# Optimization experiments

Hardware: AMD Instinct MI355X
Metric: run time of the kernel (lower is better)

## Reference

```python
import jax, jax.numpy as jnp
import numpy as np

HEADS = 16

def setup_inputs() -> dict:
    key = jax.random.key(0)
    k1, k2, k3 = jax.random.split(key, 3)
    B, S, D = 4, 2048, 1024
    x = jax.random.normal(k1, (B, S, D), dtype=jnp.float32)
    w_qkv = jax.random.normal(k2, (D, 3 * D), dtype=jnp.float32) * (D ** -0.5)
    w_out = jax.random.normal(k3, (D, D), dtype=jnp.float32) * (D ** -0.5)
    return {"x": x, "w_qkv": w_qkv, "w_out": w_out}

def reference(x, w_qkv, w_out):
    B, S, D = x.shape
    H = HEADS
    hd = D // H
    qkv = jnp.einsum("bsd,de->bse", x, w_qkv)  # [B,S,3D]
    q, k, v = jnp.split(qkv, 3, axis=-1)
    # [B,S,D] -> [B,H,S,hd]
    q = q.reshape(B, S, H, hd).transpose(0, 2, 1, 3)
    k = k.reshape(B, S, H, hd).transpose(0, 2, 1, 3)
    v = v.reshape(B, S, H, hd).transpose(0, 2, 1, 3)
    scores = jnp.einsum("bhqd,bhkd->bhqk", q, k) / jnp.sqrt(jnp.float32(hd))
    attn = jax.nn.softmax(scores, axis=-1)
    out = jnp.einsum("bhqk,bhkd->bhqd", attn, v)  # [B,H,S,hd]
    out = out.transpose(0, 2, 1, 3).reshape(B, S, D)
    return jnp.einsum("bsd,de->bse", out, w_out)
```

## Files before the change

### kernel.cpp

```cpp
#include <hip/hip_runtime.h>

typedef __bf16 bf16;
typedef __bf16 bfx8 __attribute__((ext_vector_type(8)));
typedef __bf16 bfx4 __attribute__((ext_vector_type(4)));
typedef float f32x4 __attribute__((ext_vector_type(4)));

#define MFMA_BF16 __builtin_amdgcn_mfma_f32_16x16x32_bf16

static constexpr int Bq = 4, Sq = 2048, Dq = 1024, Hq = 16, HDq = 64;
static constexpr int Mq = Bq * Sq;
static constexpr int D3 = 3 * Dq;
static constexpr int NQK = 2 * Dq;
static constexpr float L2E = 1.4426950408889634f;
static constexpr float QSC = 0.125f * L2E;

typedef const __attribute__((address_space(1))) void* gas1;
typedef __attribute__((address_space(3))) void* las3;

__device__ __forceinline__ void gload_lds16(const bf16* g, bf16* l) {
    __builtin_amdgcn_global_load_lds((gas1)g, (las3)l, 16, 0, 0);
}

__device__ __forceinline__ float fast_exp2(float x) {
    return __builtin_amdgcn_exp2f(x);
}

__global__ __launch_bounds__(256) void prep(const float* __restrict__ x,
                                            const float* __restrict__ w_qkv,
                                            const float* __restrict__ w_out,
                                            bf16* __restrict__ x_bf,
                                            bf16* __restrict__ wqkvT,
                                            bf16* __restrict__ woutT) {
    __shared__ float tile[32][33];
    int bid = blockIdx.x, tid = threadIdx.x;
    if (bid < 8192) {
        int i = (bid * 256 + tid) * 4;
        float4 v = *(const float4*)(x + i);
        bfx4 r;
        r[0] = (bf16)v.x; r[1] = (bf16)v.y; r[2] = (bf16)v.z; r[3] = (bf16)v.w;
        *(bfx4*)(x_bf + i) = r;
        return;
    }
    const float* in; bf16* out; int R, C, blk;
    if (bid < 8192 + 3072) { blk = bid - 8192;  in = w_qkv; out = wqkvT; R = Dq; C = D3; }
    else                   { blk = bid - 11264; in = w_out; out = woutT; R = Dq; C = Dq; }
    int tx = tid & 31, ty = tid >> 5;
    int nbx = C / 32;
    int c0 = (blk % nbx) * 32, r0 = (blk / nbx) * 32;
    for (int j = 0; j < 32; j += 8)
        tile[ty + j][tx] = in[(size_t)(r0 + ty + j) * C + c0 + tx];
    __syncthreads();
    for (int j = 0; j < 32; j += 8)
        out[(size_t)(c0 + ty + j) * R + r0 + tx] = (bf16)tile[tx][ty + j];
}

__device__ __forceinline__ int ldsb(int d, int s) {
    return d * 256 + ((((s >> 3) ^ (d & 15)) << 4) | ((s & 7) * 2));
}

__device__ __forceinline__ void stage_tile(const bf16* A, const bf16* Bt,
                                           bf16* As, bf16* Bs,
                                           int m0, int n0, int K, int k0, int tid) {
    #pragma unroll
    for (int i = 0; i < 4; i++) {
        int c = i * 256 + tid;
        int row = c >> 3;
        int ch = (c & 7) ^ (row & 7);
        gload_lds16(A + (size_t)(m0 + row) * K + k0 + ch * 8, As + c * 8);
        gload_lds16(Bt + (size_t)(n0 + row) * K + k0 + ch * 8, Bs + c * 8);
    }
}

template <bool OUT_F32, bool QSCALE, bool VSPLIT>
__global__ __launch_bounds__(256) void gemm_bt(const bf16* __restrict__ A,
                                               const bf16* __restrict__ Bt,
                                               void* __restrict__ Cout,
                                               bf16* __restrict__ Vout,
                                               int M, int N, int K) {
    __shared__ bf16 smem[4 * 8192];
    int m0 = blockIdx.y * 128;
    int n0 = blockIdx.x * 128;
    int tid = threadIdx.x;
    int lane = tid & 63, wave = tid >> 6;
    int quad = lane >> 4, l16 = lane & 15;
    int wr = wave >> 1, wc = wave & 1;
    int sw = l16 & 7;

    f32x4 acc[4][4] = {};

    stage_tile(A, Bt, smem, smem + 8192, m0, n0, K, 0, tid);
    asm volatile("s_waitcnt vmcnt(0)" ::: "memory");
    __builtin_amdgcn_s_barrier();

    int nt = K >> 6;
    #pragma unroll 1
    for (int t = 0; t < nt; t++) {
        int cur = t & 1;
        if (t + 1 < nt)
            stage_tile(A, Bt, smem + (cur ^ 1) * 16384, smem + (cur ^ 1) * 16384 + 8192,
                       m0, n0, K, (t + 1) * 64, tid);
        const bf16* As = smem + cur * 16384;
        const bf16* Bs = As + 8192;
        #pragma unroll
        for (int s = 0; s < 2; s++) {
            bfx8 af[4], bfr[4];
            #pragma unroll
            for (int i = 0; i < 4; i++)
                af[i] = *(const bfx8*)(As + (wr * 64 + i * 16 + l16) * 64 +
                                       ((s * 4 + quad) ^ sw) * 8);
            #pragma unroll
            for (int j = 0; j < 4; j++)
                bfr[j] = *(const bfx8*)(Bs + (wc * 64 + j * 16 + l16) * 64 +
                                        ((s * 4 + quad) ^ sw) * 8);
            #pragma unroll
            for (int i = 0; i < 4; i++)
                #pragma unroll
                for (int j = 0; j < 4; j++)
                    acc[i][j] = MFMA_BF16(af[i], bfr[j], acc[i][j], 0, 0, 0);
        }
        asm volatile("s_waitcnt vmcnt(0)" ::: "memory");
        __builtin_amdgcn_s_barrier();
    }

    if (VSPLIT && n0 >= NQK) {
        #pragma unroll
        for (int i = 0; i < 4; i++)
            #pragma unroll
            for (int j = 0; j < 4; j++) {
                int d = wc * 64 + j * 16 + l16;
                int s0 = wr * 64 + i * 16 + quad * 4;
                bfx4 pv;
                #pragma unroll
                for (int r = 0; r < 4; r++) pv[r] = (bf16)acc[i][j][r];
                *(bfx4*)((char*)smem + ldsb(d, s0)) = pv;
            }
        __syncthreads();
        int b = m0 >> 11, st = m0 & (Sq - 1), d0 = n0 - NQK;
        int g = (lane >> 3) & 1, t8 = lane & 7;
        int ss = g * 64 + (t8 >> 2) * 32 + (t8 & 3) * 4;
        #pragma unroll
        for (int rep = 0; rep < 8; rep++) {
            int d = wave * 4 + (lane >> 4) + rep * 16;
            bfx4 lo = *(const bfx4*)((char*)smem + ldsb(d, ss));
            bfx4 hi = *(const bfx4*)((char*)smem + ldsb(d, ss + 16));
            bfx8 o8;
            #pragma unroll
            for (int r = 0; r < 4; r++) { o8[r] = lo[r]; o8[4 + r] = hi[r]; }
            *(bfx8*)(Vout + ((size_t)b * Dq + d0 + d) * Sq + st + g * 64 + t8 * 8) = o8;
        }
        return;
    }

    #pragma unroll
    for (int i = 0; i < 4; i++)
        #pragma unroll
        for (int j = 0; j < 4; j++) {
            int col = n0 + wc * 64 + j * 16 + l16;
            int cstride = VSPLIT ? NQK : N;
            float scale = (QSCALE && col < Dq) ? QSC : 1.0f;
            #pragma unroll
            for (int r = 0; r < 4; r++) {
                int row = m0 + wr * 64 + i * 16 + quad * 4 + r;
                if (OUT_F32)
                    ((float*)Cout)[(size_t)row * cstride + col] = acc[i][j][r];
                else
                    ((bf16*)Cout)[(size_t)row * cstride + col] = (bf16)(acc[i][j][r] * scale);
            }
        }
}

__global__ __launch_bounds__(256, 4) void attn_kernel(const bf16* __restrict__ qkv,
                                                      const bf16* __restrict__ Vt,
                                                      bf16* __restrict__ out) {
    __shared__ bf16 Ks[3][64 * 64];
    __shared__ bf16 Vs[2][64 * 64];

    int bid = blockIdx.x;
    int qc = (bid >> 3) & 15;
    int head = ((bid >> 7) << 3) | (bid & 7);
    int h = head & 15, b = head >> 4;
    int tid = threadIdx.x;
    int lane = tid & 63, wave = tid >> 6;
    int quad = lane >> 4, l16 = lane & 15;
    int sw = l16 & 7;

    size_t base = (size_t)b * Sq * NQK;
    const bf16* Kbase = qkv + base + Dq + h * HDq;
    const bf16* Vbase = Vt + ((size_t)b * Dq + h * HDq) * Sq;
    int q0 = qc * 128 + wave * 32;

    bfx8 qf[2][2];
    #pragma unroll
    for (int qt = 0; qt < 2; qt++)
        #pragma unroll
        for (int s = 0; s < 2; s++)
            qf[qt][s] = *(const bfx8*)(qkv + base + (size_t)(q0 + qt * 16 + l16) * NQK +
                                       h * HDq + s * 32 + quad * 8);

    bfx8 ones;
    #pragma unroll
    for (int j = 0; j < 8; j++) ones[j] = (bf16)1.0f;

    f32x4 oacc[2][4] = {};
    f32x4 lacc[2] = {};

    int c0 = tid, c1 = tid + 256;
    int r0 = c0 >> 3, ch0 = (c0 & 7) ^ (r0 & 7);
    int r1 = c1 >> 3, ch1 = (c1 & 7) ^ (r1 & 7);

    bf16 *kC = Ks[0], *kN = Ks[1], *kF = Ks[2];
    bf16 *vC = Vs[0], *vN = Vs[1];

    gload_lds16(Kbase + (size_t)r0 * NQK + ch0 * 8, kC + c0 * 8);
    gload_lds16(Kbase + (size_t)r1 * NQK + ch1 * 8, kC + c1 * 8);
    gload_lds16(Vbase + (size_t)r0 * Sq + ch0 * 8, vC + c0 * 8);
    gload_lds16(Vbase + (size_t)r1 * Sq + ch1 * 8, vC + c1 * 8);
    gload_lds16(Kbase + (size_t)(64 + r0) * NQK + ch0 * 8, kN + c0 * 8);
    gload_lds16(Kbase + (size_t)(64 + r1) * NQK + ch1 * 8, kN + c1 * 8);

    #pragma unroll 1
    for (int i = 0; i < 32; i++) {
        if (i < 31) asm volatile("s_waitcnt vmcnt(2)" ::: "memory");
        else        asm volatile("s_waitcnt vmcnt(0)" ::: "memory");
        __builtin_amdgcn_s_barrier();
        if (i + 1 < 32) {
            int k0 = (i + 1) * 64;
            gload_lds16(Vbase + (size_t)r0 * Sq + k0 + ch0 * 8, vN + c0 * 8);
            gload_lds16(Vbase + (size_t)r1 * Sq + k0 + ch1 * 8, vN + c1 * 8);
        }
        if (i + 2 < 32) {
            int k0 = (i + 2) * 64;
            gload_lds16(Kbase + (size_t)(k0 + r0) * NQK + ch0 * 8, kF + c0 * 8);
            gload_lds16(Kbase + (size_t)(k0 + r1) * NQK + ch1 * 8, kF + c1 * 8);
        }
        const bf16* K_ = kC;
        const bf16* V_ = vC;

        #pragma unroll
        for (int hf = 0; hf < 2; hf++) {
            bfx8 kf[2][2];
            #pragma unroll
            for (int tp = 0; tp < 2; tp++) {
                int krow = ((2 * hf + tp) * 16 + l16) * 64;
                kf[tp][0] = *(const bfx8*)(K_ + krow + (quad ^ sw) * 8);
                kf[tp][1] = *(const bfx8*)(K_ + krow + ((4 + quad) ^ sw) * 8);
            }

            bfx8 pf[2];
            #pragma unroll
            for (int qt = 0; qt < 2; qt++) {
                f32x4 s0 = {}, s1 = {};
                s0 = MFMA_BF16(kf[0][0], qf[qt][0], s0, 0, 0, 0);
                s0 = MFMA_BF16(kf[0][1], qf[qt][1], s0, 0, 0, 0);
                s1 = MFMA_BF16(kf[1][0], qf[qt][0], s1, 0, 0, 0);
                s1 = MFMA_BF16(kf[1][1], qf[qt][1], s1, 0, 0, 0);
                bfx8 p;
                #pragma unroll
                for (int r = 0; r < 4; r++) {
                    p[r]     = (bf16)fast_exp2(s0[r]);
                    p[4 + r] = (bf16)fast_exp2(s1[r]);
                }
                pf[qt] = p;
                lacc[qt] = MFMA_BF16(pf[qt], ones, lacc[qt], 0, 0, 0);
            }

            #pragma unroll
            for (int nt = 0; nt < 4; nt++) {
                bfx8 vf = *(const bfx8*)(V_ + (nt * 16 + l16) * 64 +
                                         ((hf * 4 + quad) ^ sw) * 8);
                oacc[0][nt] = MFMA_BF16(pf[0], vf, oacc[0][nt], 0, 0, 0);
                oacc[1][nt] = MFMA_BF16(pf[1], vf, oacc[1][nt], 0, 0, 0);
            }
        }

        bf16* kt = kC; kC = kN; kN = kF; kF = kt;
        bf16* vt = vC; vC = vN; vN = vt;
    }

    #pragma unroll
    for (int qt = 0; qt < 2; qt++)
        #pragma unroll
        for (int r = 0; r < 4; r++) {
            int row = q0 + qt * 16 + quad * 4 + r;
            float inv = 1.0f / lacc[qt][r];
            #pragma unroll
            for (int nt = 0; nt < 4; nt++)
                out[((size_t)b * Sq + row) * Dq + h * HDq + nt * 16 + l16] =
                    (bf16)(oacc[qt][nt][r] * inv);
        }
}

extern "C" void kernel_launch(void* const* d_in, const int* in_sizes, int n_in,
                              void* d_out, int out_size, void* d_ws, size_t ws_size,
                              hipStream_t stream) {
    const float* x     = (const float*)d_in[0];
    const float* w_qkv = (const float*)d_in[1];
    const float* w_out = (const float*)d_in[2];
    float* out = (float*)d_out;

    char* ws = (char*)d_ws;
    bf16* x_bf   = (bf16*)ws;
    bf16* wqkvT  = (bf16*)(ws + 16777216);
    bf16* woutT  = (bf16*)(ws + 16777216 + 6291456);
    bf16* qkv2   = (bf16*)(ws + 25165824);
    bf16* Vt     = (bf16*)(ws + 25165824 + 33554432);
    bf16* attn   = x_bf;

    prep<<<8192 + 3072 + 1024, 256, 0, stream>>>(x, w_qkv, w_out, x_bf, wqkvT, woutT);

    gemm_bt<false, true, true><<<dim3(D3 / 128, Mq / 128), 256, 0, stream>>>(
        x_bf, wqkvT, qkv2, Vt, Mq, D3, Dq);

    attn_kernel<<<1024, 256, 0, stream>>>(qkv2, Vt, attn);

    gemm_bt<true, false, false><<<dim3(Dq / 128, Mq / 128), 256, 0, stream>>>(
        attn, woutT, out, nullptr, Mq, Dq, Dq);
}
```

Baseline: 231.8 us.

## Add 256x256-tile 8-wave pipelined GEMM kernel for QKV projection

Replaces the 128x128 QKV projection GEMM with a dedicated 256x256-tile, 512-thread kernel. It double-buffers LDS with global_load_lds, interleaves staging of the next K-tile with MFMA quarter-blocks under barriers, and raises MFMA priority with setprio. The V transpose epilogue and Q scaling are moved into the new kernel, and the generic GEMM is simplified. Larger tiles give more data reuse per load, at the cost of fewer blocks (384) on the chip and a lot of barriers per K step.

```diff
diff --git a/kernel.cpp b/kernel.cpp
--- a/kernel.cpp
+++ b/kernel.cpp
@@ -58,6 +58,145 @@
     return d * 256 + ((((s >> 3) ^ (d & 15)) << 4) | ((s & 7) * 2));
 }
 
+#define BAR256 __builtin_amdgcn_s_barrier()
+#define LGKM0  do { asm volatile("s_waitcnt lgkmcnt(0)" ::: "memory"); \
+                    __builtin_amdgcn_sched_barrier(0); } while (0)
+#define LDA256(BUF, MH) { \
+    const bf16* pA_ = smem + (BUF) * 16384 + wr * 8192 + ((MH) * 64 + l16) * 64; \
+    _Pragma("unroll") for (int mi_ = 0; mi_ < 4; mi_++) { \
+        af[mi_][0] = *(const bfx8*)(pA_ + mi_ * 1024 + ((quad ^ sw) * 8)); \
+        af[mi_][1] = *(const bfx8*)(pA_ + mi_ * 1024 + (((4 + quad) ^ sw) * 8)); } }
+#define LDB256(DST, BUF, NH) { \
+    const bf16* pB_ = smem + 32768 + (BUF) * 16384 + (wc >> 1) * 8192 + \
+                      (((wc & 1) * 64 + (NH) * 32 + l16) * 64); \
+    _Pragma("unroll") for (int nj_ = 0; nj_ < 2; nj_++) { \
+        DST[nj_][0] = *(const bfx8*)(pB_ + nj_ * 1024 + ((quad ^ sw) * 8)); \
+        DST[nj_][1] = *(const bfx8*)(pB_ + nj_ * 1024 + (((4 + quad) ^ sw) * 8)); } }
+#define MMA16(MH, NH, BB) { \
+    __builtin_amdgcn_s_setprio(1); \
+    _Pragma("unroll") for (int mi_ = 0; mi_ < 4; mi_++) \
+    _Pragma("unroll") for (int nj_ = 0; nj_ < 2; nj_++) { \
+        acc[(MH)*4+mi_][(NH)*2+nj_] = \
+            MFMA_BF16(af[mi_][0], BB[nj_][0], acc[(MH)*4+mi_][(NH)*2+nj_], 0, 0, 0); \
+        acc[(MH)*4+mi_][(NH)*2+nj_] = \
+            MFMA_BF16(af[mi_][1], BB[nj_][1], acc[(MH)*4+mi_][(NH)*2+nj_], 0, 0, 0); } \
+    __builtin_amdgcn_s_setprio(0); }
+
+__global__ __launch_bounds__(512, 2) void gemm256_qkv(const bf16* __restrict__ A,
+                                                      const bf16* __restrict__ Bt,
+                                                      bf16* __restrict__ Cqk,
+                                                      bf16* __restrict__ Vout) {
+    __shared__ bf16 smem[65536];
+    int n0 = blockIdx.x * 256;
+    int m0 = blockIdx.y * 256;
+    int tid = threadIdx.x;
+    int lane = tid & 63, wave = tid >> 6;
+    int quad = lane >> 4, l16 = lane & 15;
+    int wr = wave >> 2, wc = wave & 3;
+    int sw = l16 & 7;
+
+    int cs0 = tid, cs1 = tid + 512;
+    int rsA = cs0 >> 3, ccA = (cs0 & 7) ^ (rsA & 7);
+    int rsB = cs1 >> 3, ccB = (cs1 & 7) ^ (rsB & 7);
+
+    auto stgA = [&](int buf, int half, int kt) {
+        bf16* d = smem + buf * 16384 + half * 8192;
+        const bf16* s = A + (size_t)(m0 + half * 128) * Dq + kt * 64;
+        gload_lds16(s + (size_t)rsA * Dq + ccA * 8, d + cs0 * 8);
+        gload_lds16(s + (size_t)rsB * Dq + ccB * 8, d + cs1 * 8);
+    };
+    auto stgB = [&](int buf, int half, int kt) {
+        bf16* d = smem + 32768 + buf * 16384 + half * 8192;
+        const bf16* s = Bt + (size_t)(n0 + half * 128) * Dq + kt * 64;
+        gload_lds16(s + (size_t)rsA * Dq + ccA * 8, d + cs0 * 8);
+        gload_lds16(s + (size_t)rsB * Dq + ccB * 8, d + cs1 * 8);
+    };
+
+    f32x4 acc[8][4] = {};
+    bfx8 af[4][2], bb0[2][2], bb1[2][2];
+
+    stgA(0, 0, 0); stgA(0, 1, 0); stgB(0, 0, 0); stgB(0, 1, 0);
+    stgB(1, 0, 1); stgA(1, 0, 1);
+    asm volatile("s_waitcnt vmcnt(4)" ::: "memory");
+    BAR256;
+
+    #pragma unroll 1
+    for (int j = 0; j < 8; j++) {
+        int t1 = 2 * j + 1, t2 = 2 * j + 2, t3 = 2 * j + 3;
+        bool st = (j < 7);
+        LDA256(0, 0); LDB256(bb0, 0, 0);
+        stgA(1, 1, t1);
+        BAR256; LGKM0; MMA16(0, 0, bb0); BAR256;
+        LDB256(bb1, 0, 1);
+        stgB(1, 1, t1);
+        BAR256; LGKM0; MMA16(0, 1, bb1); BAR256;
+        LDA256(0, 1);
+        if (st) stgB(0, 0, t2);
+        BAR256; LGKM0; MMA16(1, 1, bb1); BAR256;
+        if (st) stgA(0, 0, t2);
+        BAR256; LGKM0; MMA16(1, 0, bb0);
+        if (st) asm volatile("s_waitcnt vmcnt(4)" ::: "memory");
+        else    asm volatile("s_waitcnt vmcnt(0)" ::: "memory");
+        BAR256;
+        LDA256(1, 0); LDB256(bb0, 1, 0);
+        if (st) stgA(0, 1, t2);
+        BAR256; LGKM0; MMA16(0, 0, bb0); BAR256;
+        LDB256(bb1, 1, 1);
+        if (st) stgB(0, 1, t2);
+        BAR256; LGKM0; MMA16(0, 1, bb1); BAR256;
+        LDA256(1, 1);
+        if (st) stgB(1, 0, t3);
+        BAR256; LGKM0; MMA16(1, 1, bb1); BAR256;
+        if (st) stgA(1, 0, t3);
+        BAR256; LGKM0; MMA16(1, 0, bb0);
+        if (st) asm volatile("s_waitcnt vmcnt(4)" ::: "memory");
+        else    asm volatile("s_waitcnt vmcnt(0)" ::: "memory");
+        BAR256;
+    }
+
+    if (n0 >= NQK) {
+        bf16* sl = smem + wave * 8192;
+        #pragma unroll
+        for (int i = 0; i < 8; i++)
+            #pragma unroll
+            for (int jj = 0; jj < 4; jj++) {
+                int dd = jj * 16 + l16;
+                int ss = i * 16 + quad * 4;
+                bfx4 pv;
+                #pragma unroll
+                for (int r = 0; r < 4; r++) pv[r] = (bf16)acc[i][jj][r];
+                *(bfx4*)((char*)sl + ldsb(dd, ss)) = pv;
+            }
+        int b = m0 >> 11, st_ = (m0 & (Sq - 1)) + wr * 128;
+        int d0 = n0 - NQK + wc * 64;
+        int g = (lane >> 3) & 1, t8 = lane & 7;
+        int ssr = g * 64 + (t8 >> 2) * 32 + (t8 & 3) * 4;
+        #pragma unroll
+        for (int rep = 0; rep < 16; rep++) {
+            int d = rep * 4 + (lane >> 4);
+            bfx4 lo = *(const bfx4*)((char*)sl + ldsb(d, ssr));
+            bfx4 hi = *(const bfx4*)((char*)sl + ldsb(d, ssr + 16));
+            bfx8 o8;
+            #pragma unroll
+            for (int r = 0; r < 4; r++) { o8[r] = lo[r]; o8[4 + r] = hi[r]; }
+            *(bfx8*)(Vout + ((size_t)b * Dq + d0 + d) * Sq + st_ + g * 64 + t8 * 8) = o8;
+        }
+        return;
+    }
+
+    #pragma unroll
+    for (int i = 0; i < 8; i++)
+        #pragma unroll
+        for (int jj = 0; jj < 4; jj++) {
+            int col = n0 + wc * 64 + jj * 16 + l16;
+            float scale = (col < Dq) ? QSC : 1.0f;
+            int row0 = m0 + wr * 128 + i * 16 + quad * 4;
+            #pragma unroll
+            for (int r = 0; r < 4; r++)
+                Cqk[(size_t)(row0 + r) * NQK + col] = (bf16)(acc[i][jj][r] * scale);
+        }
+}
+
 __device__ __forceinline__ void stage_tile(const bf16* A, const bf16* Bt,
                                            bf16* As, bf16* Bs,
                                            int m0, int n0, int K, int k0, int tid) {
@@ -71,11 +210,10 @@
     }
 }
 
-template <bool OUT_F32, bool QSCALE, bool VSPLIT>
+template <bool OUT_F32>
 __global__ __launch_bounds__(256) void gemm_bt(const bf16* __restrict__ A,
                                                const bf16* __restrict__ Bt,
                                                void* __restrict__ Cout,
-                                               bf16* __restrict__ Vout,
                                                int M, int N, int K) {
     __shared__ bf16 smem[4 * 8192];
     int m0 = blockIdx.y * 128;
@@ -122,49 +260,18 @@
         __builtin_amdgcn_s_barrier();
     }
 
-    if (VSPLIT && n0 >= NQK) {
-        #pragma unroll
-        for (int i = 0; i < 4; i++)
-            #pragma unroll
-            for (int j = 0; j < 4; j++) {
-                int d = wc * 64 + j * 16 + l16;
-                int s0 = wr * 64 + i * 16 + quad * 4;
-                bfx4 pv;
-                #pragma unroll
-                for (int r = 0; r < 4; r++) pv[r] = (bf16)acc[i][j][r];
-                *(bfx4*)((char*)smem + ldsb(d, s0)) = pv;
-            }
-        __syncthreads();
-        int b = m0 >> 11, st = m0 & (Sq - 1), d0 = n0 - NQK;
-        int g = (lane >> 3) & 1, t8 = lane & 7;
-        int ss = g * 64 + (t8 >> 2) * 32 + (t8 & 3) * 4;
-        #pragma unroll
-        for (int rep = 0; rep < 8; rep++) {
-            int d = wave * 4 + (lane >> 4) + rep * 16;
-            bfx4 lo = *(const bfx4*)((char*)smem + ldsb(d, ss));
-            bfx4 hi = *(const bfx4*)((char*)smem + ldsb(d, ss + 16));
-            bfx8 o8;
-            #pragma unroll
-            for (int r = 0; r < 4; r++) { o8[r] = lo[r]; o8[4 + r] = hi[r]; }
-            *(bfx8*)(Vout + ((size_t)b * Dq + d0 + d) * Sq + st + g * 64 + t8 * 8) = o8;
-        }
-        return;
-    }
-
     #pragma unroll
     for (int i = 0; i < 4; i++)
         #pragma unroll
         for (int j = 0; j < 4; j++) {
             int col = n0 + wc * 64 + j * 16 + l16;
-            int cstride = VSPLIT ? NQK : N;
-            float scale = (QSCALE && col < Dq) ? QSC : 1.0f;
             #pragma unroll
             for (int r = 0; r < 4; r++) {
                 int row = m0 + wr * 64 + i * 16 + quad * 4 + r;
                 if (OUT_F32)
-                    ((float*)Cout)[(size_t)row * cstride + col] = acc[i][j][r];
+                    ((float*)Cout)[(size_t)row * N + col] = acc[i][j][r];
                 else
-                    ((bf16*)Cout)[(size_t)row * cstride + col] = (bf16)(acc[i][j][r] * scale);
+                    ((bf16*)Cout)[(size_t)row * N + col] = (bf16)acc[i][j][r];
             }
         }
 }
@@ -308,11 +415,10 @@
 
     prep<<<8192 + 3072 + 1024, 256, 0, stream>>>(x, w_qkv, w_out, x_bf, wqkvT, woutT);
 
-    gemm_bt<false, true, true><<<dim3(D3 / 128, Mq / 128), 256, 0, stream>>>(
-        x_bf, wqkvT, qkv2, Vt, Mq, D3, Dq);
+    gemm256_qkv<<<dim3(D3 / 256, Mq / 256), 512, 0, stream>>>(x_bf, wqkvT, qkv2, Vt);
 
     attn_kernel<<<1024, 256, 0, stream>>>(qkv2, Vt, attn);
 
-    gemm_bt<true, false, false><<<dim3(Dq / 128, Mq / 128), 256, 0, stream>>>(
-        attn, woutT, out, nullptr, Mq, Dq, Dq);
-}
+    gemm_bt<true><<<dim3(Dq / 128, Mq / 128), 256, 0, stream>>>(
+        attn, woutT, out, Mq, Dq, Dq);
+}
```

New measurement: 242.7 us. 4.7% more time.
